# Kernel optimization log

Measured on AMD Instinct MI355X. Metric: run time of the kernel, lower is better.

## Reference

```python
import jax, jax.numpy as jnp
import numpy as np

B, N, D = 2, 2048, 1024
H, DH = 16, 64
EPS = 1e-5


def _layernorm(t, g, b):
    m = jnp.mean(t, axis=-1, keepdims=True)
    v = jnp.mean(jnp.square(t - m), axis=-1, keepdims=True)
    return (t - m) * jax.lax.rsqrt(v + EPS) * g + b


def setup_inputs() -> dict:
    key = jax.random.key(0)
    ks = jax.random.split(key, 4)
    return {
        "x": jax.random.normal(ks[0], (B, N, D), dtype=jnp.float32),
        "ln_g": jnp.ones((D,), jnp.float32),
        "ln_b": jnp.zeros((D,), jnp.float32),
        "lnc_g": jnp.ones((D,), jnp.float32),
        "lnc_b": jnp.zeros((D,), jnp.float32),
        "Wq": jax.random.normal(ks[1], (D, H * DH), jnp.float32) * 0.02,
        "Wkv": jax.random.normal(ks[2], (D, 2 * H * DH), jnp.float32) * 0.02,
        "Wo": jax.random.normal(ks[3], (H * DH, D), jnp.float32) * 0.02,
    }


def reference(x, ln_g, ln_b, lnc_g, lnc_b, Wq, Wkv, Wo):
    scale = DH ** (-0.5)
    xn = _layernorm(x, ln_g, ln_b)          # self-attn: context = x
    cn = _layernorm(x, lnc_g, lnc_b)
    q = xn @ Wq                              # [b, n, h*d]
    kv = cn @ Wkv
    k, v = jnp.split(kv, 2, axis=-1)
    # b n (h d) -> b h n d
    q = q.reshape(B, N, H, DH).transpose(0, 2, 1, 3)
    k = k.reshape(B, N, H, DH).transpose(0, 2, 1, 3)
    v = v.reshape(B, N, H, DH).transpose(0, 2, 1, 3)
    sim = jnp.einsum("bhnd,bhmd->bhnm", q, k) * scale
    neg = -jnp.finfo(sim.dtype).max
    causal = jnp.tril(jnp.ones((N, N), dtype=bool))  # allow j <= i
    sim = jnp.where(causal[None, None], sim, neg)
    attn = jax.nn.softmax(sim.astype(jnp.float32), axis=-1)
    out = jnp.einsum("bhnm,bhmd->bhnd", attn, v)
    out = out.transpose(0, 2, 1, 3).reshape(B, N, H * DH)
    return out @ Wo
```

## Files before the change

### kernel.cpp

```cpp
#include <hip/hip_runtime.h>
#include <hip/hip_bf16.h>

#define B_  2
#define N_  2048
#define D_  1024
#define H_  16
#define DH_ 64
#define BN_ROWS (B_ * N_)
#define EPS_ 1e-5f
#define QKV_N 3072

typedef __attribute__((ext_vector_type(8))) short bf16x8_t;
typedef __attribute__((ext_vector_type(4))) float f32x4_t;

typedef const unsigned int __attribute__((address_space(1)))* gas_ptr;
typedef unsigned int __attribute__((address_space(3)))* las_ptr;

__device__ __forceinline__ void async16(const unsigned short* g, unsigned short* l) {
    __builtin_amdgcn_global_load_lds((gas_ptr)g, (las_ptr)l, 16, 0, 0);
}

__device__ __forceinline__ unsigned short f2bf(float f) {
    unsigned int u = __float_as_uint(f);
    unsigned int r = u + 0x7FFFu + ((u >> 16) & 1u);
    return (unsigned short)(r >> 16);
}

__device__ __forceinline__ unsigned int pk2bf(float a, float b) {
    __hip_bfloat162 t = __float22bfloat162_rn(float2{a, b});
    return *(unsigned int*)&t;
}

__global__ __launch_bounds__(256) void ln_dual_kernel(
    const float* __restrict__ x,
    const float* __restrict__ g1, const float* __restrict__ b1,
    const float* __restrict__ g2, const float* __restrict__ b2,
    unsigned short* __restrict__ xn, unsigned short* __restrict__ cn) {
    const int row = blockIdx.x;
    const int tid = threadIdx.x;
    const float4 v = ((const float4*)(x + (size_t)row * D_))[tid];

    float s  = v.x + v.y + v.z + v.w;
    float s2 = v.x * v.x + v.y * v.y + v.z * v.z + v.w * v.w;
    #pragma unroll
    for (int off = 32; off > 0; off >>= 1) {
        s  += __shfl_down(s,  off);
        s2 += __shfl_down(s2, off);
    }
    __shared__ float red[8];
    if ((tid & 63) == 0) { red[tid >> 6] = s; red[4 + (tid >> 6)] = s2; }
    __syncthreads();
    const float S  = red[0] + red[1] + red[2] + red[3];
    const float S2 = red[4] + red[5] + red[6] + red[7];
    const float mean = S * (1.0f / D_);
    const float var  = S2 * (1.0f / D_) - mean * mean;
    const float rstd = rsqrtf(var + EPS_);

    const float4 G1 = ((const float4*)g1)[tid];
    const float4 B1 = ((const float4*)b1)[tid];
    const float4 G2 = ((const float4*)g2)[tid];
    const float4 B2 = ((const float4*)b2)[tid];

    float nx[4] = { (v.x - mean) * rstd, (v.y - mean) * rstd,
                    (v.z - mean) * rstd, (v.w - mean) * rstd };
    ushort4 o1, o2;
    o1.x = f2bf(nx[0] * G1.x + B1.x); o1.y = f2bf(nx[1] * G1.y + B1.y);
    o1.z = f2bf(nx[2] * G1.z + B1.z); o1.w = f2bf(nx[3] * G1.w + B1.w);
    o2.x = f2bf(nx[0] * G2.x + B2.x); o2.y = f2bf(nx[1] * G2.y + B2.y);
    o2.z = f2bf(nx[2] * G2.z + B2.z); o2.w = f2bf(nx[3] * G2.w + B2.w);
    ((ushort4*)(xn + (size_t)row * D_))[tid] = o1;
    ((ushort4*)(cn + (size_t)row * D_))[tid] = o2;
}

__global__ __launch_bounds__(256) void wt_transpose_all_kernel(
    const float* __restrict__ Wq, const float* __restrict__ Wkv,
    const float* __restrict__ Wo,
    unsigned short* __restrict__ wqkvT, unsigned short* __restrict__ woT) {
    const int z = blockIdx.z;
    const float* src;
    unsigned short* dst;
    int N;
    if (z == 0)      { src = Wq;  dst = wqkvT;                        N = 1024; }
    else if (z == 1) { src = Wkv; dst = wqkvT + (size_t)1024 * 1024;  N = 2048; }
    else             { src = Wo;  dst = woT;                          N = 1024; }
    const int n0 = blockIdx.x * 32, k0 = blockIdx.y * 32;
    if (n0 >= N) return;

    __shared__ float tile[32][33];
    const int tx = threadIdx.x, ty = threadIdx.y;
    #pragma unroll
    for (int i = 0; i < 4; i++)
        tile[ty + i * 8][tx] = src[(size_t)(k0 + ty + i * 8) * N + n0 + tx];
    __syncthreads();
    #pragma unroll
    for (int i = 0; i < 4; i++)
        dst[(size_t)(n0 + ty + i * 8) * 1024 + k0 + tx] = f2bf(tile[tx][ty + i * 8]);
}

__global__ __launch_bounds__(256) void vt_transpose_kernel(
    const unsigned short* __restrict__ qkv, unsigned short* __restrict__ vt) {
    __shared__ unsigned short tile[32][33];
    const int b = blockIdx.z;
    const int n0 = blockIdx.x * 32, c0 = blockIdx.y * 32;
    const int tx = threadIdx.x, ty = threadIdx.y;
    #pragma unroll
    for (int i = 0; i < 4; i++)
        tile[ty + i * 8][tx] =
            qkv[(size_t)(b * N_ + n0 + ty + i * 8) * QKV_N + 2048 + c0 + tx];
    __syncthreads();
    #pragma unroll
    for (int i = 0; i < 4; i++)
        vt[(size_t)(b * 1024 + c0 + ty + i * 8) * N_ + n0 + tx] = tile[tx][ty + i * 8];
}

template <int BM, bool FUSED, bool BF16OUT, int MINW>
__global__ __launch_bounds__(256, MINW) void gemm_kernel(
    const unsigned short* __restrict__ A0, const unsigned short* __restrict__ A1,
    const unsigned short* __restrict__ Bt, void* __restrict__ Cv,
    int M, int N, int K) {
    constexpr int WM = BM / 2, MT = WM / 16, AI = BM / 32;
    __shared__ unsigned short As[BM * 64];
    __shared__ unsigned short Bs[128 * 64];
    const int tid = threadIdx.x, lane = tid & 63, w = tid >> 6;
    const int quad = lane >> 4, l16 = lane & 15;
    const int lr8 = lane >> 3, pg8 = lane & 7;
    const int wr = (w >> 1) * WM, wc = (w & 1) * 64;
    const int bm = blockIdx.y * BM, bn = blockIdx.x * 128;
    const unsigned short* A = (FUSED && bn >= 1024) ? A1 : A0;
    const float cscale = (FUSED && bn < 1024) ? 0.180336880111120f : 1.0f;

    f32x4_t acc[MT][4] = {};
    for (int k0 = 0; k0 < K; k0 += 64) {
        #pragma unroll
        for (int i = 0; i < AI; i++) {
            const int rb = w * (BM / 4) + i * 8;
            const int r  = rb + lr8;
            const int g  = pg8 ^ (r & 7);
            async16(&A[(size_t)(bm + r) * K + k0 + g * 8], &As[rb * 64]);
        }
        #pragma unroll
        for (int i = 0; i < 4; i++) {
            const int rb = w * 32 + i * 8;
            const int r  = rb + lr8;
            const int g  = pg8 ^ (r & 7);
            async16(&Bt[(size_t)(bn + r) * K + k0 + g * 8], &Bs[rb * 64]);
        }
        __syncthreads();
        #pragma unroll
        for (int kk = 0; kk < 64; kk += 32) {
            bf16x8_t af[MT], bfr[4];
            const int g0 = (kk >> 3) + quad;
            #pragma unroll
            for (int t = 0; t < MT; t++)
                af[t] = *(const bf16x8_t*)&As[(wr + t * 16 + l16) * 64 +
                                              ((g0 ^ (l16 & 7)) * 8)];
            #pragma unroll
            for (int t = 0; t < 4; t++)
                bfr[t] = *(const bf16x8_t*)&Bs[(wc + t * 16 + l16) * 64 +
                                               ((g0 ^ (l16 & 7)) * 8)];
            #pragma unroll
            for (int mt = 0; mt < MT; mt++)
                #pragma unroll
                for (int nt = 0; nt < 4; nt++)
                    acc[mt][nt] = __builtin_amdgcn_mfma_f32_16x16x32_bf16(
                        af[mt], bfr[nt], acc[mt][nt], 0, 0, 0);
        }
        __syncthreads();
    }
    #pragma unroll
    for (int mt = 0; mt < MT; mt++)
        #pragma unroll
        for (int nt = 0; nt < 4; nt++)
            #pragma unroll
            for (int r = 0; r < 4; r++) {
                const int row = bm + wr + mt * 16 + quad * 4 + r;
                const int col = bn + wc + nt * 16 + l16;
                if (BF16OUT)
                    ((unsigned short*)Cv)[(size_t)row * N + col] =
                        f2bf(acc[mt][nt][r] * cscale);
                else
                    ((float*)Cv)[(size_t)row * N + col] = acc[mt][nt][r];
            }
}

__global__ __launch_bounds__(256, 2) void flash_attn_kernel(
    const unsigned short* __restrict__ qkv, const unsigned short* __restrict__ vt,
    unsigned short* __restrict__ out) {
    __shared__ unsigned short Qs[64 * 64];
    __shared__ unsigned short Ks[2][64 * 64];
    __shared__ unsigned short Vts[2][64 * 64];
    __shared__ unsigned short Ps[4][16 * 72];

    const int tid = threadIdx.x, lane = tid & 63, w = tid >> 6;
    const int quad = lane >> 4, l16 = lane & 15;
    const int lr8 = lane >> 3, pg8 = lane & 7;
    const int pair = blockIdx.x & 15;
    const int bh = blockIdx.x >> 4;
    const int b = bh >> 4, h = bh & 15;

    const unsigned short* qb  = qkv + (size_t)(b * N_) * QKV_N + h * DH_;
    const unsigned short* kb  = qb + 1024;
    const unsigned short* vtb = vt + (size_t)(b * 1024 + h * DH_) * N_;

    bf16x8_t ones;
    #pragma unroll
    for (int j = 0; j < 8; j++) ones[j] = (short)0x3F80;

    for (int phase = 0; phase < 2; phase++) {
        const int qt = phase ? (31 - pair) : pair;
        const int qs = qt * 64;
        const int niter = qt + 1;

        __syncthreads();

        #pragma unroll
        for (int i = 0; i < 2; i++) {
            const int rb = w * 16 + i * 8;
            const int r  = rb + lr8;
            const int g  = pg8 ^ (r & 7);
            async16(&qb[(size_t)(qs + r) * QKV_N + g * 8], &Qs[rb * 64]);
            async16(&kb[(size_t)r * QKV_N + g * 8], &Ks[0][rb * 64]);
            async16(&vtb[(size_t)r * N_ + g * 8],   &Vts[0][rb * 64]);
        }

        f32x4_t o[4] = {};
        f32x4_t lacc = {};
        bf16x8_t qf[2];

        for (int jt = 0; jt < niter; jt++) {
            __syncthreads();

            if (jt + 1 < niter) {
                const int js = (jt + 1) * 64;
                const int bsel = (jt + 1) & 1;
                #pragma unroll
                for (int i = 0; i < 2; i++) {
                    const int rb = w * 16 + i * 8;
                    const int r  = rb + lr8;
                    const int g  = pg8 ^ (r & 7);
                    async16(&kb[(size_t)(js + r) * QKV_N + g * 8], &Ks[bsel][rb * 64]);
                    async16(&vtb[(size_t)r * N_ + js + g * 8],     &Vts[bsel][rb * 64]);
                }
            }
            const int buf = jt & 1;
            const int js = jt * 64;

            if (jt == 0) {
                #pragma unroll
                for (int k2 = 0; k2 < 2; k2++) {
                    const int g0 = k2 * 4 + quad;
                    qf[k2] = *(const bf16x8_t*)&Qs[
                        (w * 16 + l16) * 64 + (g0 ^ (l16 & 7)) * 8];
                }
            }

            f32x4_t s[4] = {};
            #pragma unroll
            for (int k2 = 0; k2 < 2; k2++) {
                const int g0 = k2 * 4 + quad;
                #pragma unroll
                for (int kt = 0; kt < 4; kt++) {
                    const bf16x8_t a = *(const bf16x8_t*)&Ks[buf][
                        (kt * 16 + l16) * 64 + (g0 ^ (l16 & 7)) * 8];
                    s[kt] = __builtin_amdgcn_mfma_f32_16x16x32_bf16(
                        a, qf[k2], s[kt], 0, 0, 0);
                }
            }

            const bool edge = (jt == niter - 1);
            #pragma unroll
            for (int kt = 0; kt < 4; kt++) {
                float p[4];
                #pragma unroll
                for (int r = 0; r < 4; r++) {
                    float sv = s[kt][r];
                    if (edge) {
                        const int key = js + kt * 16 + quad * 4 + r;
                        const int qy  = qs + w * 16 + l16;
                        if (key > qy) sv = -3e38f;
                    }
                    p[r] = exp2f(sv);
                }
                uint2 pk = { pk2bf(p[0], p[1]), pk2bf(p[2], p[3]) };
                *(uint2*)&Ps[w][l16 * 72 + kt * 16 + quad * 4] = pk;
            }

            #pragma unroll
            for (int k2 = 0; k2 < 2; k2++) {
                const int g0 = k2 * 4 + quad;
                const bf16x8_t ap = *(const bf16x8_t*)&Ps[w][
                    l16 * 72 + k2 * 32 + quad * 8];
                #pragma unroll
                for (int nt = 0; nt < 4; nt++) {
                    const bf16x8_t bv = *(const bf16x8_t*)&Vts[buf][
                        (nt * 16 + l16) * 64 + (g0 ^ (l16 & 7)) * 8];
                    o[nt] = __builtin_amdgcn_mfma_f32_16x16x32_bf16(
                        ap, bv, o[nt], 0, 0, 0);
                }
                lacc = __builtin_amdgcn_mfma_f32_16x16x32_bf16(
                    ap, ones, lacc, 0, 0, 0);
            }
        }

        #pragma unroll
        for (int r = 0; r < 4; r++) {
            const float inv = 1.0f / lacc[r];
            const int query = qs + w * 16 + quad * 4 + r;
            const int row = b * N_ + query;
            #pragma unroll
            for (int nt = 0; nt < 4; nt++) {
                const int col = h * DH_ + nt * 16 + l16;
                out[(size_t)row * (H_ * DH_) + col] = f2bf(o[nt][r] * inv);
            }
        }
    }
}

extern "C" void kernel_launch(void* const* d_in, const int* in_sizes, int n_in,
                              void* d_out, int out_size, void* d_ws, size_t ws_size,
                              hipStream_t stream) {
    const float* x     = (const float*)d_in[0];
    const float* ln_g  = (const float*)d_in[1];
    const float* ln_b  = (const float*)d_in[2];
    const float* lnc_g = (const float*)d_in[3];
    const float* lnc_b = (const float*)d_in[4];
    const float* Wq    = (const float*)d_in[5];
    const float* Wkv   = (const float*)d_in[6];
    const float* Wo    = (const float*)d_in[7];

    char* ws = (char*)d_ws;
    const size_t MB = 1024 * 1024;
    unsigned short* qkv   = (unsigned short*)(ws + 0 * MB);
    unsigned short* vtbuf = (unsigned short*)(ws + 24 * MB);
    unsigned short* xn    = (unsigned short*)(ws + 32 * MB);
    unsigned short* cn    = (unsigned short*)(ws + 40 * MB);
    unsigned short* wqkvT = (unsigned short*)(ws + 48 * MB);
    unsigned short* woT   = (unsigned short*)(ws + 54 * MB);
    unsigned short* ao    = xn;

    ln_dual_kernel<<<BN_ROWS, 256, 0, stream>>>(x, ln_g, ln_b, lnc_g, lnc_b, xn, cn);

    wt_transpose_all_kernel<<<dim3(64, 32, 3), dim3(32, 8), 0, stream>>>(
        Wq, Wkv, Wo, wqkvT, woT);

    gemm_kernel<128, true, true, 3>
        <<<dim3(QKV_N / 128, BN_ROWS / 128), 256, 0, stream>>>(
        xn, cn, wqkvT, qkv, BN_ROWS, QKV_N, D_);

    vt_transpose_kernel<<<dim3(64, 32, 2), dim3(32, 8), 0, stream>>>(qkv, vtbuf);

    flash_attn_kernel<<<B_ * H_ * 16, 256, 0, stream>>>(qkv, vtbuf, ao);

    gemm_kernel<64, false, false, 2>
        <<<dim3(D_ / 128, BN_ROWS / 64), 256, 0, stream>>>(
        ao, nullptr, woT, (float*)d_out, BN_ROWS, D_, H_ * DH_);
}
```

Baseline: 198.9 us.

## Fuse V-transpose into QKV GEMM epilogue, merge LN and weight transpose kernels

The QKV GEMM epilogue now writes V directly in a tiled transposed layout ([b][ktile][col][64]), so the separate V-transpose kernel disappears. Flash attention reads that blocked layout with contiguous 64-element rows. LayerNorm and the weight transpose/convert are merged into one launch to remove a kernel launch. The attention block index is also remapped, and the QKV GEMM occupancy hint drops from 3 to 2. The intent is fewer launches and less memory traffic, at the cost of a more specialised epilogue that may write with poorer coalescing.

```diff
diff --git a/kernel.cpp b/kernel.cpp
--- a/kernel.cpp
+++ b/kernel.cpp
@@ -31,93 +31,79 @@
     return *(unsigned int*)&t;
 }
 
-__global__ __launch_bounds__(256) void ln_dual_kernel(
+__global__ __launch_bounds__(256) void ln_wt_kernel(
     const float* __restrict__ x,
     const float* __restrict__ g1, const float* __restrict__ b1,
     const float* __restrict__ g2, const float* __restrict__ b2,
-    unsigned short* __restrict__ xn, unsigned short* __restrict__ cn) {
-    const int row = blockIdx.x;
-    const int tid = threadIdx.x;
-    const float4 v = ((const float4*)(x + (size_t)row * D_))[tid];
-
-    float s  = v.x + v.y + v.z + v.w;
-    float s2 = v.x * v.x + v.y * v.y + v.z * v.z + v.w * v.w;
-    #pragma unroll
-    for (int off = 32; off > 0; off >>= 1) {
-        s  += __shfl_down(s,  off);
-        s2 += __shfl_down(s2, off);
-    }
-    __shared__ float red[8];
-    if ((tid & 63) == 0) { red[tid >> 6] = s; red[4 + (tid >> 6)] = s2; }
-    __syncthreads();
-    const float S  = red[0] + red[1] + red[2] + red[3];
-    const float S2 = red[4] + red[5] + red[6] + red[7];
-    const float mean = S * (1.0f / D_);
-    const float var  = S2 * (1.0f / D_) - mean * mean;
-    const float rstd = rsqrtf(var + EPS_);
-
-    const float4 G1 = ((const float4*)g1)[tid];
-    const float4 B1 = ((const float4*)b1)[tid];
-    const float4 G2 = ((const float4*)g2)[tid];
-    const float4 B2 = ((const float4*)b2)[tid];
-
-    float nx[4] = { (v.x - mean) * rstd, (v.y - mean) * rstd,
-                    (v.z - mean) * rstd, (v.w - mean) * rstd };
-    ushort4 o1, o2;
-    o1.x = f2bf(nx[0] * G1.x + B1.x); o1.y = f2bf(nx[1] * G1.y + B1.y);
-    o1.z = f2bf(nx[2] * G1.z + B1.z); o1.w = f2bf(nx[3] * G1.w + B1.w);
-    o2.x = f2bf(nx[0] * G2.x + B2.x); o2.y = f2bf(nx[1] * G2.y + B2.y);
-    o2.z = f2bf(nx[2] * G2.z + B2.z); o2.w = f2bf(nx[3] * G2.w + B2.w);
-    ((ushort4*)(xn + (size_t)row * D_))[tid] = o1;
-    ((ushort4*)(cn + (size_t)row * D_))[tid] = o2;
-}
-
-__global__ __launch_bounds__(256) void wt_transpose_all_kernel(
     const float* __restrict__ Wq, const float* __restrict__ Wkv,
     const float* __restrict__ Wo,
+    unsigned short* __restrict__ xn, unsigned short* __restrict__ cn,
     unsigned short* __restrict__ wqkvT, unsigned short* __restrict__ woT) {
-    const int z = blockIdx.z;
-    const float* src;
-    unsigned short* dst;
-    int N;
-    if (z == 0)      { src = Wq;  dst = wqkvT;                        N = 1024; }
-    else if (z == 1) { src = Wkv; dst = wqkvT + (size_t)1024 * 1024;  N = 2048; }
-    else             { src = Wo;  dst = woT;                          N = 1024; }
-    const int n0 = blockIdx.x * 32, k0 = blockIdx.y * 32;
-    if (n0 >= N) return;
-
-    __shared__ float tile[32][33];
-    const int tx = threadIdx.x, ty = threadIdx.y;
-    #pragma unroll
-    for (int i = 0; i < 4; i++)
-        tile[ty + i * 8][tx] = src[(size_t)(k0 + ty + i * 8) * N + n0 + tx];
-    __syncthreads();
-    #pragma unroll
-    for (int i = 0; i < 4; i++)
-        dst[(size_t)(n0 + ty + i * 8) * 1024 + k0 + tx] = f2bf(tile[tx][ty + i * 8]);
-}
-
-__global__ __launch_bounds__(256) void vt_transpose_kernel(
-    const unsigned short* __restrict__ qkv, unsigned short* __restrict__ vt) {
-    __shared__ unsigned short tile[32][33];
-    const int b = blockIdx.z;
-    const int n0 = blockIdx.x * 32, c0 = blockIdx.y * 32;
-    const int tx = threadIdx.x, ty = threadIdx.y;
-    #pragma unroll
-    for (int i = 0; i < 4; i++)
-        tile[ty + i * 8][tx] =
-            qkv[(size_t)(b * N_ + n0 + ty + i * 8) * QKV_N + 2048 + c0 + tx];
-    __syncthreads();
-    #pragma unroll
-    for (int i = 0; i < 4; i++)
-        vt[(size_t)(b * 1024 + c0 + ty + i * 8) * N_ + n0 + tx] = tile[tx][ty + i * 8];
-}
-
-template <int BM, bool FUSED, bool BF16OUT, int MINW>
-__global__ __launch_bounds__(256, MINW) void gemm_kernel(
+    const int bid = blockIdx.x;
+    const int tid = threadIdx.x;
+
+    if (bid < BN_ROWS) {
+        const int row = bid;
+        const float4 v = ((const float4*)(x + (size_t)row * D_))[tid];
+
+        float s  = v.x + v.y + v.z + v.w;
+        float s2 = v.x * v.x + v.y * v.y + v.z * v.z + v.w * v.w;
+        #pragma unroll
+        for (int off = 32; off > 0; off >>= 1) {
+            s  += __shfl_down(s,  off);
+            s2 += __shfl_down(s2, off);
+        }
+        __shared__ float red[8];
+        if ((tid & 63) == 0) { red[tid >> 6] = s; red[4 + (tid >> 6)] = s2; }
+        __syncthreads();
+        const float S  = red[0] + red[1] + red[2] + red[3];
+        const float S2 = red[4] + red[5] + red[6] + red[7];
+        const float mean = S * (1.0f / D_);
+        const float var  = S2 * (1.0f / D_) - mean * mean;
+        const float rstd = rsqrtf(var + EPS_);
+
+        const float4 G1 = ((const float4*)g1)[tid];
+        const float4 B1 = ((const float4*)b1)[tid];
+        const float4 G2 = ((const float4*)g2)[tid];
+        const float4 B2 = ((const float4*)b2)[tid];
+
+        float nx[4] = { (v.x - mean) * rstd, (v.y - mean) * rstd,
+                        (v.z - mean) * rstd, (v.w - mean) * rstd };
+        ushort4 o1, o2;
+        o1.x = f2bf(nx[0] * G1.x + B1.x); o1.y = f2bf(nx[1] * G1.y + B1.y);
+        o1.z = f2bf(nx[2] * G1.z + B1.z); o1.w = f2bf(nx[3] * G1.w + B1.w);
+        o2.x = f2bf(nx[0] * G2.x + B2.x); o2.y = f2bf(nx[1] * G2.y + B2.y);
+        o2.z = f2bf(nx[2] * G2.z + B2.z); o2.w = f2bf(nx[3] * G2.w + B2.w);
+        ((ushort4*)(xn + (size_t)row * D_))[tid] = o1;
+        ((ushort4*)(cn + (size_t)row * D_))[tid] = o2;
+    } else {
+        const int zz = bid - BN_ROWS;
+        const float* src;
+        unsigned short* dst;
+        int N, t;
+        if (zz < 1024)      { src = Wq;  dst = wqkvT;                       N = 1024; t = zz; }
+        else if (zz < 3072) { src = Wkv; dst = wqkvT + (size_t)1024 * 1024; N = 2048; t = zz - 1024; }
+        else                { src = Wo;  dst = woT;                         N = 1024; t = zz - 3072; }
+        const int nb = N / 32;
+        const int n0 = (t % nb) * 32, k0 = (t / nb) * 32;
+
+        __shared__ float tile[32][33];
+        const int tx = tid & 31, ty = tid >> 5;
+        #pragma unroll
+        for (int i = 0; i < 4; i++)
+            tile[ty + i * 8][tx] = src[(size_t)(k0 + ty + i * 8) * N + n0 + tx];
+        __syncthreads();
+        #pragma unroll
+        for (int i = 0; i < 4; i++)
+            dst[(size_t)(n0 + ty + i * 8) * 1024 + k0 + tx] = f2bf(tile[tx][ty + i * 8]);
+    }
+}
+
+template <int BM, bool FUSED, bool BF16OUT>
+__global__ __launch_bounds__(256, 2) void gemm_kernel(
     const unsigned short* __restrict__ A0, const unsigned short* __restrict__ A1,
     const unsigned short* __restrict__ Bt, void* __restrict__ Cv,
-    int M, int N, int K) {
+    unsigned short* __restrict__ vt, int M, int N, int K) {
     constexpr int WM = BM / 2, MT = WM / 16, AI = BM / 32;
     __shared__ unsigned short As[BM * 64];
     __shared__ unsigned short Bs[128 * 64];
@@ -167,6 +153,26 @@
         }
         __syncthreads();
     }
+
+    if (FUSED && bn >= 2048) {
+        const int seq0 = bm + wr;
+        const int bq = seq0 >> 11;
+        const int kt = (seq0 & (N_ - 1)) >> 6;
+        #pragma unroll
+        for (int nt = 0; nt < 4; nt++) {
+            const int c = (bn - 2048) + wc + nt * 16 + l16;
+            unsigned short* dst =
+                vt + (((size_t)(bq * 32 + kt) * 1024) + c) * 64;
+            #pragma unroll
+            for (int mt = 0; mt < 4; mt++) {
+                uint2 v2 = { pk2bf(acc[mt][nt][0], acc[mt][nt][1]),
+                             pk2bf(acc[mt][nt][2], acc[mt][nt][3]) };
+                *(uint2*)&dst[mt * 16 + quad * 4] = v2;
+            }
+        }
+        return;
+    }
+
     #pragma unroll
     for (int mt = 0; mt < MT; mt++)
         #pragma unroll
@@ -194,13 +200,14 @@
     const int tid = threadIdx.x, lane = tid & 63, w = tid >> 6;
     const int quad = lane >> 4, l16 = lane & 15;
     const int lr8 = lane >> 3, pg8 = lane & 7;
-    const int pair = blockIdx.x & 15;
-    const int bh = blockIdx.x >> 4;
+    const int bid = blockIdx.x;
+    const int bh   = (bid & 7) * 4 + ((bid >> 3) & 3);
+    const int pair = bid >> 5;
     const int b = bh >> 4, h = bh & 15;
 
     const unsigned short* qb  = qkv + (size_t)(b * N_) * QKV_N + h * DH_;
     const unsigned short* kb  = qb + 1024;
-    const unsigned short* vtb = vt + (size_t)(b * 1024 + h * DH_) * N_;
+    const unsigned short* vtb = vt + ((size_t)(b * 32) * 1024 + h * 64) * 64;
 
     bf16x8_t ones;
     #pragma unroll
@@ -220,7 +227,7 @@
             const int g  = pg8 ^ (r & 7);
             async16(&qb[(size_t)(qs + r) * QKV_N + g * 8], &Qs[rb * 64]);
             async16(&kb[(size_t)r * QKV_N + g * 8], &Ks[0][rb * 64]);
-            async16(&vtb[(size_t)r * N_ + g * 8],   &Vts[0][rb * 64]);
+            async16(&vtb[(size_t)r * 64 + g * 8],   &Vts[0][rb * 64]);
         }
 
         f32x4_t o[4] = {};
@@ -239,7 +246,8 @@
                     const int r  = rb + lr8;
                     const int g  = pg8 ^ (r & 7);
                     async16(&kb[(size_t)(js + r) * QKV_N + g * 8], &Ks[bsel][rb * 64]);
-                    async16(&vtb[(size_t)r * N_ + js + g * 8],     &Vts[bsel][rb * 64]);
+                    async16(&vtb[((size_t)(jt + 1) * 1024 + r) * 64 + g * 8],
+                            &Vts[bsel][rb * 64]);
                 }
             }
             const int buf = jt & 1;
@@ -338,20 +346,16 @@
     unsigned short* woT   = (unsigned short*)(ws + 54 * MB);
     unsigned short* ao    = xn;
 
-    ln_dual_kernel<<<BN_ROWS, 256, 0, stream>>>(x, ln_g, ln_b, lnc_g, lnc_b, xn, cn);
-
-    wt_transpose_all_kernel<<<dim3(64, 32, 3), dim3(32, 8), 0, stream>>>(
-        Wq, Wkv, Wo, wqkvT, woT);
-
-    gemm_kernel<128, true, true, 3>
+    ln_wt_kernel<<<8192, 256, 0, stream>>>(
+        x, ln_g, ln_b, lnc_g, lnc_b, Wq, Wkv, Wo, xn, cn, wqkvT, woT);
+
+    gemm_kernel<128, true, true>
         <<<dim3(QKV_N / 128, BN_ROWS / 128), 256, 0, stream>>>(
-        xn, cn, wqkvT, qkv, BN_ROWS, QKV_N, D_);
-
-    vt_transpose_kernel<<<dim3(64, 32, 2), dim3(32, 8), 0, stream>>>(qkv, vtbuf);
+        xn, cn, wqkvT, qkv, vtbuf, BN_ROWS, QKV_N, D_);
 
     flash_attn_kernel<<<B_ * H_ * 16, 256, 0, stream>>>(qkv, vtbuf, ao);
 
-    gemm_kernel<64, false, false, 2>
+    gemm_kernel<64, false, false>
         <<<dim3(D_ / 128, BN_ROWS / 64), 256, 0, stream>>>(
-        ao, nullptr, woT, (float*)d_out, BN_ROWS, D_, H_ * DH_);
-}
+        ao, nullptr, woT, (float*)d_out, nullptr, BN_ROWS, D_, H_ * DH_);
+}
```

New measurement: 179.5 us. 9.8% less time.
